# Performance work log

Measured on AMD Instinct MI355X. Metric: run time of the kernel, lower is better.

The kernel has to match this reference:

```python
import jax, jax.numpy as jnp
import numpy as np

B, T, D, M, L = 4, 2048, 256, 128, 16
P = M * L  # max_pair_cnt


def setup_inputs() -> dict:
    key = jax.random.key(0)
    ks = jax.random.split(key, 11)
    head = jax.random.normal(ks[0], (B, P, T), jnp.float32) * 0.05
    tail = jax.random.normal(ks[1], (B, P, T), jnp.float32) * 0.05
    x = jax.random.normal(ks[2], (B, T, D), jnp.float32)
    coref_mention_position = jax.random.uniform(ks[3], (B, M, T), jnp.float32)
    lab = jax.random.uniform(ks[4], (B, P, 2), jnp.float32) + 1e-3
    coref_label = lab / lab.sum(-1, keepdims=True)  # already-softmaxed target
    coref_label_mask = jax.random.randint(ks[5], (B, P), 0, 2).astype(bool)
    lens = jnp.full((B, M), L, jnp.int32)  # uniform segment lengths
    w1 = jax.random.normal(ks[6], (3 * D, D), jnp.float32) / np.sqrt(3 * D).astype(np.float32)
    b1 = jnp.zeros((D,), jnp.float32)
    w2 = jax.random.normal(ks[7], (D, 2), jnp.float32) / np.sqrt(D).astype(np.float32)
    b2 = jnp.zeros((2,), jnp.float32)
    return {"head": head, "tail": tail, "lens": lens, "x": x,
            "coref_mention_position": coref_mention_position,
            "coref_label": coref_label, "coref_label_mask": coref_label_mask,
            "w1": w1, "b1": b1, "w2": w2, "b2": b2}


def reference(head, tail, lens, x, coref_mention_position, coref_label,
              coref_label_mask, w1, b1, w2, b2):
    # bmm-based gather of mention reps: [B,P,T] @ [B,T,D] -> [B,P,D]
    head_rep = jnp.einsum('bpt,btd->bpd', head, x)
    tail_rep = jnp.einsum('bpt,btd->bpd', tail, x)
    feat = jnp.concatenate([head_rep, tail_rep, head_rep * tail_rep], axis=-1)
    logits = jax.nn.relu(feat @ w1 + b1) @ w2 + b2  # [B,P,2]

    # ragged split_n_pad -> per-mention top-1 select (uniform lens == L -> reshape)
    scores = logits[..., 1].reshape(B, M, L)            # [B,M,L]
    max_idx = jnp.argmax(scores, axis=-1)               # [B,M]
    max_val = jnp.max(scores, axis=-1)                  # [B,M] (raw logit, as in source)
    tail_seg = tail_rep.reshape(B, M, L, D)
    sel = jnp.take_along_axis(tail_seg, max_idx[:, :, None, None], axis=2)[:, :, 0, :]
    coref_rep_m = sel * max_val[:, :, None]             # [B,M,D]

    # scatter-bmm merge back into sequence: [B,T,M] @ [B,M,D] -> [B,T,D]
    coref_rep = jnp.einsum('bmt,bmd->btd', coref_mention_position, coref_rep_m)
    output = x + coref_rep

    # KLDivLoss(reduction='mean') over masked pairs
    logq = jax.nn.log_softmax(logits, axis=-1)
    lab = coref_label
    pw = jnp.where(lab > 0, lab * jnp.log(jnp.maximum(lab, 1e-38)), 0.0) - lab * logq
    n = jnp.sum(coref_label_mask).astype(jnp.float32)
    loss = jnp.where(coref_label_mask[..., None], pw, 0.0).sum() / (n * 2.0)
    return output, loss
```

## Files before the change

kernel.cpp:

```cpp
#include <hip/hip_runtime.h>
#include <hip/hip_bf16.h>
#include <stdint.h>

#define TAU 0.35f

typedef __attribute__((ext_vector_type(8))) short bf16x8;
typedef __attribute__((ext_vector_type(4))) float f32x4;

__device__ __forceinline__ unsigned short f2bf(float f) {
  __bf16 h = (__bf16)f;
  return __builtin_bit_cast(unsigned short, h);
}
__device__ __forceinline__ float bf2f(unsigned short u) {
  unsigned int v = ((unsigned int)u) << 16;
  return __builtin_bit_cast(float, v);
}
__device__ __forceinline__ void async_copy16(const void* g, void* l) {
  __builtin_amdgcn_global_load_lds(
      (const __attribute__((address_space(1))) unsigned int*)g,
      (__attribute__((address_space(3))) unsigned int*)l, 16, 0, 0);
}
__device__ __forceinline__ float rdlane(float v, int l) {
  return __builtin_bit_cast(float,
      __builtin_amdgcn_readlane(__builtin_bit_cast(int, v), l));
}

__global__ __launch_bounds__(256) void k_prep(
    const float* __restrict__ x, const float* __restrict__ w1,
    const float* __restrict__ b2,
    unsigned short* __restrict__ xt, unsigned short* __restrict__ w1t,
    float* __restrict__ logits, int* __restrict__ njobs,
    float* __restrict__ featws) {
  __shared__ float tileS[64][65];
  __shared__ float tx[64][132];
  int bx = blockIdx.x, tid = threadIdx.x;
  if (bx == 0 && tid < 4) njobs[tid] = 0;
  if (bx < 64) {
    int i = bx * 256 + tid;
    logits[i] = b2[i & 1];
  }
  {
    float4 z = {0.f, 0.f, 0.f, 0.f};
    for (int i = bx * 256 + tid; i < 1048576; i += 304 * 256)
      ((float4*)featws)[i] = z;
  }
  if (bx < 256) {
    int b = bx >> 6, kc = (bx >> 1) & 31, dh = bx & 1;
    const float* src = x + ((size_t)b * 2048 + (size_t)kc * 64) * 256 + dh * 128;
#pragma unroll
    for (int p = 0; p < 8; ++p) {
      int idx = p * 256 + tid;
      int row = idx >> 5, f4 = idx & 31;
      *(float4*)&tx[row][f4 * 4] = *(const float4*)&src[(size_t)row * 256 + f4 * 4];
    }
    __syncthreads();
    unsigned short* dst = xt + ((size_t)(b * 32 + kc)) * 16384 + dh * 1024;
#pragma unroll
    for (int p = 0; p < 4; ++p) {
      int idx = p * 256 + tid;
      int d0 = idx & 127, k8 = idx >> 7;
      bf16x8 v;
#pragma unroll
      for (int j = 0; j < 8; ++j) v[j] = (short)f2bf(tx[k8 * 8 + j][d0]);
      *(bf16x8*)&dst[(size_t)k8 * 2048 + d0 * 8] = v;
    }
  } else {
    int wt = bx - 256;
    int k6 = wt >> 2, n6 = wt & 3;
    int j = tid & 63, i0 = tid >> 6;
    const float* src = w1 + ((size_t)k6 * 64) * 256 + n6 * 64;
    for (int i = i0; i < 64; i += 4) tileS[i][j] = src[(size_t)i * 256 + j];
    __syncthreads();
    unsigned short* dst = w1t + ((size_t)n6 * 64) * 768 + k6 * 64;
    for (int r = i0; r < 64; r += 4) dst[(size_t)r * 768 + j] = f2bf(tileS[j][r]);
  }
}

__global__ __launch_bounds__(512, 8) void k_gemm_rep(
    const float* __restrict__ head, const float* __restrict__ tail,
    const unsigned short* __restrict__ xt,
    float* __restrict__ hrep, float* __restrict__ trep) {
  __shared__ unsigned short As[2][1024];
  __shared__ unsigned short Bs[2][8192];
  int bx = blockIdx.x;
  int b = bx >> 7, mt = bx & 127;
  const float* Asrc = ((mt < 64) ? head : tail) +
                      ((size_t)(b * 2048 + (mt & 63) * 32)) * 2048;
  float* Crep = (mt < 64) ? hrep : trep;
  const unsigned short* Bsrc = xt + (size_t)b * 524288;

  int tid = threadIdx.x, lane = tid & 63, w = tid >> 6;
  int rg = w & 1, cg = w >> 1;
  int l4 = lane >> 4, l15 = lane & 15;

  int arow = tid >> 2, ak8 = tid & 3;
  const float* aptr = Asrc + (size_t)arow * 2048 + ak8 * 8;
  int awi = (ak8 * 32 + arow) * 8;

  const unsigned short* bg = Bsrc + tid * 8;

  int aoff = (l4 * 32 + rg * 16 + l15) * 8;
  int boff[4];
#pragma unroll
  for (int ct = 0; ct < 4; ++ct)
    boff[ct] = (l4 * 256 + cg * 64 + ct * 16 + l15) * 8;

  f32x4 acc[4];
#pragma unroll
  for (int ct = 0; ct < 4; ++ct) acc[ct] = (f32x4){0.f, 0.f, 0.f, 0.f};

  float4 av0, av1;
  auto STAGEB = [&](int buf) {
#pragma unroll
    for (int a = 0; a < 2; ++a)
      async_copy16(bg + (size_t)a * 4096, &Bs[buf][(tid + a * 512) * 8]);
    bg += 8192;
  };
  auto LOADA = [&]() {
    const float4* ap = (const float4*)aptr;
    av0 = ap[0]; av1 = ap[1];
    aptr += 32;
  };
  auto WRITEA = [&](int buf) {
    bf16x8 p;
    p[0] = (short)f2bf(av0.x); p[1] = (short)f2bf(av0.y);
    p[2] = (short)f2bf(av0.z); p[3] = (short)f2bf(av0.w);
    p[4] = (short)f2bf(av1.x); p[5] = (short)f2bf(av1.y);
    p[6] = (short)f2bf(av1.z); p[7] = (short)f2bf(av1.w);
    *(bf16x8*)&As[buf][awi] = p;
  };
  auto MMA = [&](int buf) {
    const unsigned short* A_ = As[buf];
    const unsigned short* B_ = Bs[buf];
    bf16x8 a0 = *(const bf16x8*)&A_[aoff];
#pragma unroll
    for (int ct = 0; ct < 4; ++ct) {
      bf16x8 bb = *(const bf16x8*)&B_[boff[ct]];
      acc[ct] = __builtin_amdgcn_mfma_f32_16x16x32_bf16(a0, bb, acc[ct], 0, 0, 0);
    }
  };

  STAGEB(0);
  if (tid < 128) { LOADA(); WRITEA(0); }
  __syncthreads();

  for (int it = 0; it < 64; ++it) {
    int cur = it & 1, nxt = cur ^ 1;
    if (it < 63) {
      STAGEB(nxt);
      if (tid < 128) LOADA();
    }
    MMA(cur);
    if (it < 63 && tid < 128) WRITEA(nxt);
    __syncthreads();
  }

  size_t prow = (size_t)b * 2048 + (size_t)(mt & 63) * 32 + rg * 16 + (l4 << 2);
  int cb = cg * 64 + l15;
#pragma unroll
  for (int ct = 0; ct < 4; ++ct)
#pragma unroll
    for (int i = 0; i < 4; ++i)
      Crep[(prow + i) * 256 + cb + ct * 16] = acc[ct][i];
}

__global__ __launch_bounds__(256) void k_feat(
    const float* __restrict__ hrep, const float* __restrict__ trep,
    unsigned short* __restrict__ featbf) {
  int gid = blockIdx.x * 256 + threadIdx.x;
  int p = gid >> 6, d0 = (gid & 63) * 4;
  float4 h4 = *(const float4*)&hrep[(size_t)p * 256 + d0];
  float4 t4 = *(const float4*)&trep[(size_t)p * 256 + d0];
  ushort4 a, bb, c;
  a.x = f2bf(h4.x); a.y = f2bf(h4.y); a.z = f2bf(h4.z); a.w = f2bf(h4.w);
  bb.x = f2bf(t4.x); bb.y = f2bf(t4.y); bb.z = f2bf(t4.z); bb.w = f2bf(t4.w);
  c.x = f2bf(h4.x * t4.x); c.y = f2bf(h4.y * t4.y);
  c.z = f2bf(h4.z * t4.z); c.w = f2bf(h4.w * t4.w);
  *(ushort4*)&featbf[(size_t)p * 768 + d0] = a;
  *(ushort4*)&featbf[(size_t)p * 768 + 256 + d0] = bb;
  *(ushort4*)&featbf[(size_t)p * 768 + 512 + d0] = c;
}

__global__ __launch_bounds__(256, 4) void k_gemm_mlp(
    const unsigned short* __restrict__ featb, const unsigned short* __restrict__ w1t,
    const float* __restrict__ b1, const float* __restrict__ w2,
    float* __restrict__ logits) {
  __shared__ unsigned short As[2][4096], Bs[2][4096];
  int bx = blockIdx.x;
  int ntile = bx >> 7;
  int mtile = bx & 127;
  int tid = threadIdx.x, lane = tid & 63, w = tid >> 6;

  const unsigned short* ag[2];
  const unsigned short* bgp[2];
  int dofs[2];
#pragma unroll
  for (int a = 0; a < 2; ++a) {
    int rowofs = a * 8 + (lane >> 3);
    int k8 = (lane & 7) ^ (rowofs & 7);
    ag[a] = featb + (size_t)(mtile * 64 + w * 16 + rowofs) * 768 + k8 * 8;
    bgp[a] = w1t + (size_t)(ntile * 64 + w * 16 + rowofs) * 768 + k8 * 8;
    dofs[a] = (w * 128 + a * 64 + lane) * 8;
  }
  int sw0 = (lane >> 4) ^ (lane & 7);
  int sw1 = (4 + (lane >> 4)) ^ (lane & 7);
  int arowc = (w * 16 + (lane & 15)) * 8;
  int colc[4];
#pragma unroll
  for (int ct = 0; ct < 4; ++ct) colc[ct] = (ct * 16 + (lane & 15)) * 8;

  f32x4 acc[4];
#pragma unroll
  for (int ct = 0; ct < 4; ++ct) acc[ct] = (f32x4){0.f, 0.f, 0.f, 0.f};

#pragma unroll
  for (int a = 0; a < 2; ++a) {
    async_copy16(ag[a], &As[0][dofs[a]]); ag[a] += 64;
    async_copy16(bgp[a], &Bs[0][dofs[a]]); bgp[a] += 64;
  }
  __syncthreads();

  for (int it = 0; it < 12; ++it) {
    int cur = it & 1, nxt = cur ^ 1;
    if (it < 11) {
#pragma unroll
      for (int a = 0; a < 2; ++a) {
        async_copy16(ag[a], &As[nxt][dofs[a]]); ag[a] += 64;
        async_copy16(bgp[a], &Bs[nxt][dofs[a]]); bgp[a] += 64;
      }
    }
    const unsigned short* A_ = As[cur];
    const unsigned short* B_ = Bs[cur];
    bf16x8 a0 = *(const bf16x8*)&A_[(arowc + sw0) * 8];
    bf16x8 a1 = *(const bf16x8*)&A_[(arowc + sw1) * 8];
#pragma unroll
    for (int ct = 0; ct < 4; ++ct) {
      bf16x8 b0 = *(const bf16x8*)&B_[(colc[ct] + sw0) * 8];
      acc[ct] = __builtin_amdgcn_mfma_f32_16x16x32_bf16(a0, b0, acc[ct], 0, 0, 0);
    }
#pragma unroll
    for (int ct = 0; ct < 4; ++ct) {
      bf16x8 b1 = *(const bf16x8*)&B_[(colc[ct] + sw1) * 8];
      acc[ct] = __builtin_amdgcn_mfma_f32_16x16x32_bf16(a1, b1, acc[ct], 0, 0, 0);
    }
    __syncthreads();
  }

  float bv[4], w20[4], w21[4];
#pragma unroll
  for (int ct = 0; ct < 4; ++ct) {
    int col = ntile * 64 + ct * 16 + (lane & 15);
    bv[ct] = b1[col]; w20[ct] = w2[col * 2]; w21[ct] = w2[col * 2 + 1];
  }
#pragma unroll
  for (int i = 0; i < 4; ++i) {
    float s0 = 0.f, s1 = 0.f;
#pragma unroll
    for (int ct = 0; ct < 4; ++ct) {
      float r = fmaxf(acc[ct][i] + bv[ct], 0.f);
      s0 += r * w20[ct]; s1 += r * w21[ct];
    }
#pragma unroll
    for (int off = 1; off < 16; off <<= 1) {
      s0 += __shfl_xor(s0, off); s1 += __shfl_xor(s1, off);
    }
    if ((lane & 15) == 0) {
      int row = mtile * 64 + w * 16 + ((lane >> 4) << 2) + i;
      atomicAdd(&logits[row * 2], s0);
      atomicAdd(&logits[row * 2 + 1], s1);
    }
  }
}

__global__ __launch_bounds__(512) void k_select_loss(
    const float* __restrict__ logits, int* __restrict__ idxv,
    float* __restrict__ mval, int* __restrict__ cmask,
    int* __restrict__ njobs, int* __restrict__ jobs,
    const float* __restrict__ lab, const unsigned char* __restrict__ mask,
    float* __restrict__ out_loss) {
  __shared__ float rs[512], rc[512];
  int tid = threadIdx.x;
  {
    int q = tid;
    int base = q * 16;
    float s[16];
#pragma unroll
    for (int i = 0; i < 16; ++i) s[i] = logits[(size_t)(base + i) * 2 + 1];
    float best = s[0]; int bi = 0;
#pragma unroll
    for (int i = 1; i < 16; ++i) if (s[i] > best) { best = s[i]; bi = i; }
    int msk = 0, cnt = 0;
#pragma unroll
    for (int i = 0; i < 16; ++i) if (s[i] > best - TAU) { msk |= 1 << i; ++cnt; }
    idxv[q] = bi; mval[q] = best;
    if (cnt > 1) {
      cmask[q] = msk;
      int bb = q >> 7;
      for (int i = 0; i < 16; ++i)
        if ((msk >> i) & 1) {
          int j = atomicAdd(&njobs[bb], 1);
          jobs[bb * 2048 + j] = base + i;
        }
    } else cmask[q] = 0;
  }
  float sum = 0.f, cnt = 0.f;
  for (int p = tid; p < 8192; p += 512) {
    float l0 = logits[(size_t)p * 2], l1 = logits[(size_t)p * 2 + 1];
    float a0 = lab[(size_t)p * 2], a1 = lab[(size_t)p * 2 + 1];
    float mx = fmaxf(l0, l1);
    float lse = mx + logf(expf(l0 - mx) + expf(l1 - mx));
    float pw = 0.f;
    if (a0 > 0.f) pw += a0 * logf(fmaxf(a0, 1e-38f));
    if (a1 > 0.f) pw += a1 * logf(fmaxf(a1, 1e-38f));
    pw -= a0 * (l0 - lse) + a1 * (l1 - lse);
    if (mask[p]) { sum += pw; cnt += 1.f; }
  }
  rs[tid] = sum; rc[tid] = cnt;
  __syncthreads();
  for (int s = 256; s > 0; s >>= 1) {
    if (tid < s) { rs[tid] += rs[tid + s]; rc[tid] += rc[tid + s]; }
    __syncthreads();
  }
  if (tid == 0) *out_loss = rs[0] / (rc[0] * 2.0f);
}

__global__ __launch_bounds__(1024) void k_refine_dot(
    const int* __restrict__ njobs, const int* __restrict__ jobs,
    const float* __restrict__ head, const float* __restrict__ tail,
    const float* __restrict__ x,
    float* __restrict__ featH, float* __restrict__ featT) {
  __shared__ float red[4][16][256];
  __shared__ int scode[8];
  int tid = threadIdx.x, lane = tid & 63, w = tid >> 6;
  int tg = w >> 2, dg = w & 3;
  int d = dg * 64 + lane;

  for (int gt = blockIdx.x; ; gt += gridDim.x) {
    int rem = gt, b = 0, nj = 0;
    for (; b < 4; ++b) {
      nj = njobs[b];
      int ntb = ((nj + 7) >> 3) * 8;
      if (rem < ntb) break;
      rem -= ntb;
    }
    if (b == 4) break;
    int grp = rem >> 3, tc = rem & 7;
    __syncthreads();
    if (tid < 8) scode[tid] = jobs[b * 2048 + min(grp * 8 + tid, nj - 1)];
    __syncthreads();

    int t0 = tc * 256 + tg * 64;
    float vh[8], vt[8];
#pragma unroll
    for (int j = 0; j < 8; ++j) {
      int p = scode[j] & 2047;
      size_t ro = ((size_t)(b * 2048 + p)) * 2048 + t0 + lane;
      vh[j] = head[ro]; vt[j] = tail[ro];
    }
    float ah[8] = {0.f, 0.f, 0.f, 0.f, 0.f, 0.f, 0.f, 0.f};
    float at[8] = {0.f, 0.f, 0.f, 0.f, 0.f, 0.f, 0.f, 0.f};
    const float* xp = x + (size_t)b * 524288 + (size_t)t0 * 256 + d;
#pragma unroll 8
    for (int t = 0; t < 64; ++t) {
      float xv = xp[(size_t)t * 256];
#pragma unroll
      for (int j = 0; j < 8; ++j) {
        ah[j] += rdlane(vh[j], t) * xv;
        at[j] += rdlane(vt[j], t) * xv;
      }
    }
#pragma unroll
    for (int j = 0; j < 8; ++j) {
      red[tg][j][d] = ah[j];
      red[tg][8 + j][d] = at[j];
    }
    __syncthreads();
    if (tid < 256) {
#pragma unroll
      for (int j = 0; j < 16; ++j) {
        float s = red[0][j][tid] + red[1][j][tid] + red[2][j][tid] + red[3][j][tid];
        int jj = j & 7;
        if (grp * 8 + jj < nj) {
          float* dst = (j < 8) ? featH : featT;
          atomicAdd(&dst[(size_t)scode[jj] * 256 + tid], s);
        }
      }
    }
  }
}

__global__ __launch_bounds__(1024) void k_refine_mlp(
    const int* __restrict__ njobs, const int* __restrict__ jobs,
    const float* __restrict__ featH, const float* __restrict__ featT,
    const float* __restrict__ w1, const float* __restrict__ b1,
    const float* __restrict__ w2, const float* __restrict__ b2,
    float* __restrict__ refined) {
  __shared__ float feat8[768][8];
  __shared__ float redm[4][8][256];
  __shared__ float part[8][4];
  __shared__ int scode[8];
  int tid = threadIdx.x;
  int hseg = tid >> 8, d = tid & 255;

  for (int gt = blockIdx.x; ; gt += gridDim.x) {
    int rem = gt, b = 0, nj = 0;
    for (; b < 4; ++b) {
      nj = njobs[b];
      int ntb = (nj + 7) >> 3;
      if (rem < ntb) break;
      rem -= ntb;
    }
    if (b == 4) break;
    int grp = rem;
    __syncthreads();
    if (tid < 8) scode[tid] = jobs[b * 2048 + min(grp * 8 + tid, nj - 1)];
    __syncthreads();
#pragma unroll
    for (int r = 0; r < 2; ++r) {
      int j = hseg * 2 + r;
      float h = featH[(size_t)scode[j] * 256 + d];
      float t = featT[(size_t)scode[j] * 256 + d];
      feat8[d][j] = h; feat8[256 + d][j] = t; feat8[512 + d][j] = h * t;
    }
    __syncthreads();
    float hp[8] = {0.f, 0.f, 0.f, 0.f, 0.f, 0.f, 0.f, 0.f};
    const float* w1c = w1 + (size_t)(hseg * 192) * 256 + d;
#pragma unroll 4
    for (int ii = 0; ii < 192; ++ii) {
      float wv = w1c[(size_t)ii * 256];
      float4 f0 = *(const float4*)&feat8[hseg * 192 + ii][0];
      float4 f1 = *(const float4*)&feat8[hseg * 192 + ii][4];
      hp[0] += f0.x * wv; hp[1] += f0.y * wv; hp[2] += f0.z * wv; hp[3] += f0.w * wv;
      hp[4] += f1.x * wv; hp[5] += f1.y * wv; hp[6] += f1.z * wv; hp[7] += f1.w * wv;
    }
#pragma unroll
    for (int j = 0; j < 8; ++j) redm[hseg][j][d] = hp[j];
    __syncthreads();
    if (tid < 256) {
      float w2v = w2[tid * 2 + 1], b1v = b1[tid];
#pragma unroll
      for (int j = 0; j < 8; ++j) {
        float h = b1v + redm[0][j][tid] + redm[1][j][tid] + redm[2][j][tid] + redm[3][j][tid];
        h = fmaxf(h, 0.f) * w2v;
#pragma unroll
        for (int off = 1; off < 64; off <<= 1) h += __shfl_xor(h, off);
        if ((tid & 63) == 0) part[j][tid >> 6] = h;
      }
    }
    __syncthreads();
    if (tid < 8 && grp * 8 + tid < nj)
      refined[scode[tid]] = part[tid][0] + part[tid][1] + part[tid][2] + part[tid][3] + b2[1];
  }
}

__global__ __launch_bounds__(256) void k_repm(
    const int* __restrict__ idxv, const float* __restrict__ mval,
    const int* __restrict__ cmask, const float* __restrict__ refined,
    const float* __restrict__ trep, float* __restrict__ repm) {
  int q = blockIdx.x, d = threadIdx.x;
  int mask = cmask[q]; int bi; float v;
  if (mask) {
    bi = -1; v = -1e30f;
    for (int i = 0; i < 16; ++i)
      if ((mask >> i) & 1) { float s = refined[q * 16 + i]; if (s > v) { v = s; bi = i; } }
  } else { bi = idxv[q]; v = mval[q]; }
  repm[(size_t)q * 256 + d] = trep[((size_t)q * 16 + bi) * 256 + d] * v;
}

__global__ __launch_bounds__(256) void k_merge(
    const float* __restrict__ cmp, const float* __restrict__ repm,
    const float* __restrict__ x, float* __restrict__ out) {
  __shared__ float cl[128 * 16];
  int bx = blockIdx.x, b = bx >> 7, t0 = (bx & 127) * 16;
  int tid = threadIdx.x;
#pragma unroll
  for (int it = 0; it < 2; ++it) {
    int f = it * 256 + tid;
    int row = f >> 2, c4 = (f & 3) * 4;
    *(float4*)&cl[row * 16 + c4] =
        *(const float4*)&cmp[((size_t)(b * 128 + row)) * 2048 + t0 + c4];
  }
  __syncthreads();
  float acc[16];
#pragma unroll
  for (int i = 0; i < 16; ++i) acc[i] = 0.f;
  int d = tid;
  for (int m = 0; m < 128; ++m) {
    float rv = repm[(size_t)(b * 128 + m) * 256 + d];
    const float4* c4p = (const float4*)&cl[m * 16];
#pragma unroll
    for (int jj = 0; jj < 4; ++jj) {
      float4 c = c4p[jj];
      acc[jj * 4] += c.x * rv; acc[jj * 4 + 1] += c.y * rv;
      acc[jj * 4 + 2] += c.z * rv; acc[jj * 4 + 3] += c.w * rv;
    }
  }
  const float* xb = x + ((size_t)(b * 2048 + t0)) * 256 + d;
  float* ob = out + ((size_t)(b * 2048 + t0)) * 256 + d;
#pragma unroll
  for (int tt = 0; tt < 16; ++tt) ob[(size_t)tt * 256] = xb[(size_t)tt * 256] + acc[tt];
}

extern "C" void kernel_launch(void* const* d_in, const int* in_sizes, int n_in,
                              void* d_out, int out_size, void* d_ws, size_t ws_size,
                              hipStream_t stream) {
  (void)in_sizes; (void)n_in; (void)out_size; (void)ws_size;
  const float* head = (const float*)d_in[0];
  const float* tail = (const float*)d_in[1];
  const float* x = (const float*)d_in[3];
  const float* cmp = (const float*)d_in[4];
  const float* lab = (const float*)d_in[5];
  const unsigned char* lmask = (const unsigned char*)d_in[6];
  const float* w1 = (const float*)d_in[7];
  const float* b1 = (const float*)d_in[8];
  const float* w2 = (const float*)d_in[9];
  const float* b2 = (const float*)d_in[10];
  float* out = (float*)d_out;

  char* ws = (char*)d_ws;
  size_t off = 0;
  auto alloc = [&](size_t bytes) -> void* {
    void* p = ws + off; off += (bytes + 255) & ~(size_t)255; return p;
  };
  unsigned short* xt = (unsigned short*)alloc(4ull * 256 * 2048 * 2);
  unsigned short* w1t = (unsigned short*)alloc(256ull * 768 * 2);
  float* hrep = (float*)alloc(8192ull * 256 * 4);
  float* trep = (float*)alloc(8192ull * 256 * 4);
  unsigned short* featb = (unsigned short*)alloc(8192ull * 768 * 2);
  float* logits = (float*)alloc(8192ull * 2 * 4);
  float* refined = (float*)alloc(8192ull * 4);
  int* idxv = (int*)alloc(512 * 4);
  float* mvalv = (float*)alloc(512 * 4);
  int* cmaskv = (int*)alloc(512 * 4);
  int* njobs = (int*)alloc(256);
  int* jobs = (int*)alloc(4 * 2048 * 4);
  float* repm = (float*)alloc(512ull * 256 * 4);
  float* featH = (float*)alloc(8192ull * 256 * 4);
  float* featT = (float*)alloc(8192ull * 256 * 4);

  k_prep<<<304, 256, 0, stream>>>(x, w1, b2, xt, w1t, logits, njobs, featH);
  k_gemm_rep<<<512, 512, 0, stream>>>(head, tail, xt, hrep, trep);
  k_feat<<<2048, 256, 0, stream>>>(hrep, trep, featb);
  k_gemm_mlp<<<512, 256, 0, stream>>>(featb, w1t, b1, w2, logits);
  k_select_loss<<<1, 512, 0, stream>>>(logits, idxv, mvalv, cmaskv, njobs, jobs,
                                       lab, lmask, out + 4ull * 2048 * 256);
  k_refine_dot<<<512, 1024, 0, stream>>>(njobs, jobs, head, tail, x, featH, featT);
  k_refine_mlp<<<128, 1024, 0, stream>>>(njobs, jobs, featH, featT, w1, b1, w2, b2, refined);
  k_repm<<<512, 256, 0, stream>>>(idxv, mvalv, cmaskv, refined, trep, repm);
  k_merge<<<512, 256, 0, stream>>>(cmp, repm, x, out);
}
```

Before: 344.2 us.

## Split rep GEMM across output-column halves with deeper K tile and swizzled A

The head/tail representation GEMM now launches twice as many blocks, each computing half of the 256 output columns, with the K step doubled to 64 so the loop runs 32 iterations. All 512 threads now load and convert A (fp32 to bf16) instead of only 128, and the A tile in LDS gets an XOR swizzle to reduce bank conflicts. This raises parallelism and spreads the A-load work, but each A row block is read from global memory twice, once per column half, which increases head/tail traffic.

Measured after the change: 344.1 us. No clear change (-0.0%).

```diff
diff --git a/kernel.cpp b/kernel.cpp
--- a/kernel.cpp
+++ b/kernel.cpp
@@ -80,85 +80,102 @@
     const float* __restrict__ head, const float* __restrict__ tail,
     const unsigned short* __restrict__ xt,
     float* __restrict__ hrep, float* __restrict__ trep) {
-  __shared__ unsigned short As[2][1024];
+  __shared__ unsigned short As[2][2048];
   __shared__ unsigned short Bs[2][8192];
   int bx = blockIdx.x;
-  int b = bx >> 7, mt = bx & 127;
+  int ch = bx >> 9;
+  int g = bx & 511;
+  int b = g >> 7, mt = g & 127;
   const float* Asrc = ((mt < 64) ? head : tail) +
                       ((size_t)(b * 2048 + (mt & 63) * 32)) * 2048;
   float* Crep = (mt < 64) ? hrep : trep;
-  const unsigned short* Bsrc = xt + (size_t)b * 524288;
+  const unsigned short* Bsrc = xt + (size_t)b * 524288 + ch * 1024;
 
   int tid = threadIdx.x, lane = tid & 63, w = tid >> 6;
   int rg = w & 1, cg = w >> 1;
   int l4 = lane >> 4, l15 = lane & 15;
 
-  int arow = tid >> 2, ak8 = tid & 3;
-  const float* aptr = Asrc + (size_t)arow * 2048 + ak8 * 8;
-  int awi = (ak8 * 32 + arow) * 8;
-
-  const unsigned short* bg = Bsrc + tid * 8;
-
-  int aoff = (l4 * 32 + rg * 16 + l15) * 8;
-  int boff[4];
-#pragma unroll
-  for (int ct = 0; ct < 4; ++ct)
-    boff[ct] = (l4 * 256 + cg * 64 + ct * 16 + l15) * 8;
-
-  f32x4 acc[4];
-#pragma unroll
-  for (int ct = 0; ct < 4; ++ct) acc[ct] = (f32x4){0.f, 0.f, 0.f, 0.f};
-
-  float4 av0, av1;
+  int arow = tid >> 4, aq4 = tid & 15;
+  const float* aptr = Asrc + (size_t)arow * 2048 + aq4 * 4;
+  int ak8 = aq4 >> 1, ahalf = aq4 & 1;
+  int awi = (((ak8 * 32 + arow) * 8 + ahalf * 4)) ^ ((ak8 & 3) << 4);
+
+  const unsigned short* bg[2];
+  int bdst[2];
+#pragma unroll
+  for (int a = 0; a < 2; ++a) {
+    int idx = a * 512 + tid;
+    int run = idx >> 7, pos = idx & 127;
+    bg[a] = Bsrc + run * 2048 + pos * 8;
+    bdst[a] = (run * 128 + pos) * 8;
+  }
+
+  int aoff[2];
+  int boff[2][2];
+#pragma unroll
+  for (int kh = 0; kh < 2; ++kh) {
+    int k8 = kh * 4 + l4;
+    aoff[kh] = (((k8 * 32 + rg * 16 + l15) * 8)) ^ ((k8 & 3) << 4);
+#pragma unroll
+    for (int ct = 0; ct < 2; ++ct)
+      boff[kh][ct] = (k8 * 128 + cg * 32 + ct * 16 + l15) * 8;
+  }
+
+  f32x4 acc[2];
+  acc[0] = (f32x4){0.f, 0.f, 0.f, 0.f};
+  acc[1] = (f32x4){0.f, 0.f, 0.f, 0.f};
+
+  float4 av;
   auto STAGEB = [&](int buf) {
 #pragma unroll
-    for (int a = 0; a < 2; ++a)
-      async_copy16(bg + (size_t)a * 4096, &Bs[buf][(tid + a * 512) * 8]);
-    bg += 8192;
+    for (int a = 0; a < 2; ++a) {
+      async_copy16(bg[a], &Bs[buf][bdst[a]]);
+      bg[a] += 16384;
+    }
   };
   auto LOADA = [&]() {
-    const float4* ap = (const float4*)aptr;
-    av0 = ap[0]; av1 = ap[1];
-    aptr += 32;
+    av = *(const float4*)aptr;
+    aptr += 64;
   };
   auto WRITEA = [&](int buf) {
-    bf16x8 p;
-    p[0] = (short)f2bf(av0.x); p[1] = (short)f2bf(av0.y);
-    p[2] = (short)f2bf(av0.z); p[3] = (short)f2bf(av0.w);
-    p[4] = (short)f2bf(av1.x); p[5] = (short)f2bf(av1.y);
-    p[6] = (short)f2bf(av1.z); p[7] = (short)f2bf(av1.w);
-    *(bf16x8*)&As[buf][awi] = p;
+    ushort4 p;
+    p.x = f2bf(av.x); p.y = f2bf(av.y); p.z = f2bf(av.z); p.w = f2bf(av.w);
+    *(ushort4*)&As[buf][awi] = p;
   };
   auto MMA = [&](int buf) {
     const unsigned short* A_ = As[buf];
     const unsigned short* B_ = Bs[buf];
-    bf16x8 a0 = *(const bf16x8*)&A_[aoff];
-#pragma unroll
-    for (int ct = 0; ct < 4; ++ct) {
-      bf16x8 bb = *(const bf16x8*)&B_[boff[ct]];
-      acc[ct] = __builtin_amdgcn_mfma_f32_16x16x32_bf16(a0, bb, acc[ct], 0, 0, 0);
+#pragma unroll
+    for (int kh = 0; kh < 2; ++kh) {
+      bf16x8 a0 = *(const bf16x8*)&A_[aoff[kh]];
+#pragma unroll
+      for (int ct = 0; ct < 2; ++ct) {
+        bf16x8 bb = *(const bf16x8*)&B_[boff[kh][ct]];
+        acc[ct] = __builtin_amdgcn_mfma_f32_16x16x32_bf16(a0, bb, acc[ct], 0, 0, 0);
+      }
     }
   };
 
   STAGEB(0);
-  if (tid < 128) { LOADA(); WRITEA(0); }
+  LOADA();
+  WRITEA(0);
   __syncthreads();
 
-  for (int it = 0; it < 64; ++it) {
+  for (int it = 0; it < 32; ++it) {
     int cur = it & 1, nxt = cur ^ 1;
-    if (it < 63) {
+    if (it < 31) {
       STAGEB(nxt);
-      if (tid < 128) LOADA();
+      LOADA();
     }
     MMA(cur);
-    if (it < 63 && tid < 128) WRITEA(nxt);
+    if (it < 31) WRITEA(nxt);
     __syncthreads();
   }
 
   size_t prow = (size_t)b * 2048 + (size_t)(mt & 63) * 32 + rg * 16 + (l4 << 2);
-  int cb = cg * 64 + l15;
-#pragma unroll
-  for (int ct = 0; ct < 4; ++ct)
+  int cb = ch * 128 + cg * 32 + l15;
+#pragma unroll
+  for (int ct = 0; ct < 2; ++ct)
 #pragma unroll
     for (int i = 0; i < 4; ++i)
       Crep[(prow + i) * 256 + cb + ct * 16] = acc[ct][i];
@@ -539,7 +556,7 @@
   float* featT = (float*)alloc(8192ull * 256 * 4);
 
   k_prep<<<304, 256, 0, stream>>>(x, w1, b2, xt, w1t, logits, njobs, featH);
-  k_gemm_rep<<<512, 512, 0, stream>>>(head, tail, xt, hrep, trep);
+  k_gemm_rep<<<1024, 512, 0, stream>>>(head, tail, xt, hrep, trep);
   k_feat<<<2048, 256, 0, stream>>>(hrep, trep, featb);
   k_gemm_mlp<<<512, 256, 0, stream>>>(featb, w1t, b1, w2, logits);
   k_select_loss<<<1, 512, 0, stream>>>(logits, idxv, mvalv, cmaskv, njobs, jobs,
```
